# Kernel optimization log

Measured on AMD Instinct MI355X. Metric: run time of the kernel, lower is better.

## Reference

```python
import jax, jax.numpy as jnp
import numpy as np

NUM_USERS = 200_000
NUM_ITEMS = 100_000
N = NUM_USERS + NUM_ITEMS
D = 32
E = 9_600_000
N_LAYERS = 3


def setup_inputs() -> dict:
    key = jax.random.key(0)
    k1, k2, k3, k4, k5 = jax.random.split(key, 5)
    rows = jax.random.randint(k1, (E,), 0, N, dtype=jnp.int32)
    cols = jax.random.randint(k2, (E,), 0, N, dtype=jnp.int32)
    # normalized-adjacency-like positive values
    vals = jax.random.uniform(k3, (E,), dtype=jnp.float32) * 0.05
    # xavier-uniform-ish embedding init
    bound = float(np.sqrt(6.0 / (NUM_USERS + D)))
    user_w = jax.random.uniform(k4, (NUM_USERS, D), dtype=jnp.float32,
                                minval=-bound, maxval=bound)
    bound_i = float(np.sqrt(6.0 / (NUM_ITEMS + D)))
    item_w = jax.random.uniform(k5, (NUM_ITEMS, D), dtype=jnp.float32,
                                minval=-bound_i, maxval=bound_i)
    return {"rows": rows, "cols": cols, "vals": vals,
            "user_w": user_w, "item_w": item_w}


def _spmm(rows, cols, vals, x):
    # A_hat @ x for COO A_hat: gather source features, scale, scatter-add to rows.
    msgs = vals[:, None] * x[cols]                 # [E, D]
    return jax.ops.segment_sum(msgs, rows, num_segments=N)  # [N, D]


def reference(rows, cols, vals, user_w, item_w):
    x0 = jnp.concatenate([user_w, item_w], axis=0)  # [N, D]
    x = x0
    acc = x0
    for _ in range(N_LAYERS):
        x = _spmm(rows, cols, vals, x)
        acc = acc + x
    x_mean = acc / (N_LAYERS + 1)                   # mean over layer stack
    users = x_mean[:NUM_USERS]
    items = x_mean[NUM_USERS:]
    return (users, items)
```

## Files before the change

### kernel.cpp

```cpp
#include <hip/hip_runtime.h>
#include <hip/hip_fp16.h>
#include <stdint.h>

#define NUM_USERS 200000
#define NUM_ITEMS 100000
#define NN (NUM_USERS + NUM_ITEMS)
#define D 32
#define NE 9600000
#define TOTAL (NN * D)

#define RPB2 128
#define B2 ((NN + RPB2 - 1) / RPB2)
#define CAP 5120

#define TPB_A 1024
#define EPT 16
#define EPB_A (TPB_A * EPT)

#define TPB_H 1024
#define EPT_H 32
#define EPB_H (TPB_H * EPT_H)
#define NB_H ((NE + EPB_H - 1) / EPB_H)

__global__ __launch_bounds__(256) void init_x_acc(
    const float4* __restrict__ user_w, const float4* __restrict__ item_w,
    ushort4* __restrict__ xh, float4* __restrict__ acc) {
    int i = blockIdx.x * 256 + threadIdx.x;
    const int total4 = TOTAL / 4;
    const int ub4 = (NUM_USERS * D) / 4;
    if (i < total4) {
        float4 v = (i < ub4) ? user_w[i] : item_w[i - ub4];
        acc[i] = v;
        ushort4 h;
        h.x = __half_as_ushort(__float2half(v.x));
        h.y = __half_as_ushort(__float2half(v.y));
        h.z = __half_as_ushort(__float2half(v.z));
        h.w = __half_as_ushort(__float2half(v.w));
        xh[i] = h;
    }
}

__global__ __launch_bounds__(TPB_H) void bucket_hist(
    const int4* __restrict__ rows4, int* __restrict__ bcounts) {
    __shared__ int hist[B2];
    int tid = threadIdx.x;
    for (int i = tid; i < B2; i += TPB_H) hist[i] = 0;
    __syncthreads();
    int base4 = blockIdx.x * (EPB_H / 4);
    #pragma unroll
    for (int k = 0; k < EPT_H / 4; ++k) {
        int i4 = base4 + k * TPB_H + tid;
        if (i4 < NE / 4) {
            int4 r = rows4[i4];
            atomicAdd(&hist[r.x >> 7], 1);
            atomicAdd(&hist[r.y >> 7], 1);
            atomicAdd(&hist[r.z >> 7], 1);
            atomicAdd(&hist[r.w >> 7], 1);
        }
    }
    __syncthreads();
    for (int b = tid; b < B2; b += TPB_H) {
        int c = hist[b];
        if (c) atomicAdd(&bcounts[b], c);
    }
}

__global__ __launch_bounds__(1024) void scan_buckets(
    const int* __restrict__ bcounts, int* __restrict__ bstart,
    int* __restrict__ bfill) {
    __shared__ int lds[1024];
    int t = threadIdx.x;
    int v[4];
    int s = 0;
    #pragma unroll
    for (int k = 0; k < 4; ++k) {
        int b = t * 4 + k;
        v[k] = (b < B2) ? bcounts[b] : 0;
        s += v[k];
    }
    lds[t] = s;
    __syncthreads();
    for (int off = 1; off < 1024; off <<= 1) {
        int u = (t >= off) ? lds[t - off] : 0;
        __syncthreads();
        lds[t] += u;
        __syncthreads();
    }
    int ex = lds[t] - s;
    #pragma unroll
    for (int k = 0; k < 4; ++k) {
        int b = t * 4 + k;
        if (b < B2) { bstart[b] = ex; bfill[b] = ex; }
        ex += v[k];
    }
    if (t == 1023) bstart[B2] = ex;
}

__global__ __launch_bounds__(TPB_A) void partition_edges(
    const int4* __restrict__ rows4, const int4* __restrict__ cols4,
    const float4* __restrict__ vals4, int* __restrict__ bfill,
    int2* __restrict__ temp) {
    __shared__ int hist[B2];
    int tid = threadIdx.x;
    for (int i = tid; i < B2; i += TPB_A) hist[i] = 0;
    __syncthreads();

    int base4 = blockIdx.x * (EPB_A / 4);
    uint32_t brank[EPT];

    #pragma unroll
    for (int k = 0; k < EPT / 4; ++k) {
        int i4 = base4 + k * TPB_A + tid;
        if (i4 < NE / 4) {
            int4 r = rows4[i4];
            uint32_t b0 = (uint32_t)r.x >> 7, b1 = (uint32_t)r.y >> 7;
            uint32_t b2 = (uint32_t)r.z >> 7, b3 = (uint32_t)r.w >> 7;
            brank[k * 4 + 0] = (b0 << 20) | (uint32_t)((r.x & 127) << 13) | (uint32_t)atomicAdd(&hist[b0], 1);
            brank[k * 4 + 1] = (b1 << 20) | (uint32_t)((r.y & 127) << 13) | (uint32_t)atomicAdd(&hist[b1], 1);
            brank[k * 4 + 2] = (b2 << 20) | (uint32_t)((r.z & 127) << 13) | (uint32_t)atomicAdd(&hist[b2], 1);
            brank[k * 4 + 3] = (b3 << 20) | (uint32_t)((r.w & 127) << 13) | (uint32_t)atomicAdd(&hist[b3], 1);
        }
    }
    __syncthreads();
    for (int b = tid; b < B2; b += TPB_A) {
        int c = hist[b];
        if (c) hist[b] = atomicAdd(&bfill[b], c);
    }
    __syncthreads();

    #pragma unroll
    for (int k = 0; k < EPT / 4; ++k) {
        int i4 = base4 + k * TPB_A + tid;
        if (i4 < NE / 4) {
            int4 c = cols4[i4];
            float4 v = vals4[i4];
            uint32_t br; int pos; int2 cv;
            br = brank[k * 4 + 0]; pos = hist[br >> 20] + (int)(br & 0x1FFFu);
            cv.x = (int)(((br >> 13) & 127u) << 19) | c.x; cv.y = __float_as_int(v.x); temp[pos] = cv;
            br = brank[k * 4 + 1]; pos = hist[br >> 20] + (int)(br & 0x1FFFu);
            cv.x = (int)(((br >> 13) & 127u) << 19) | c.y; cv.y = __float_as_int(v.y); temp[pos] = cv;
            br = brank[k * 4 + 2]; pos = hist[br >> 20] + (int)(br & 0x1FFFu);
            cv.x = (int)(((br >> 13) & 127u) << 19) | c.z; cv.y = __float_as_int(v.z); temp[pos] = cv;
            br = brank[k * 4 + 3]; pos = hist[br >> 20] + (int)(br & 0x1FFFu);
            cv.x = (int)(((br >> 13) & 127u) << 19) | c.w; cv.y = __float_as_int(v.w); temp[pos] = cv;
        }
    }
}

__global__ __launch_bounds__(256) void sort_bucket2(
    const int* __restrict__ bstart, const int2* __restrict__ temp,
    int* __restrict__ row_start, int2* __restrict__ colval) {
    __shared__ int2 stage[CAP];
    __shared__ int lstart[RPB2];
    __shared__ int lfill[RPB2];
    int b = blockIdx.x;
    int row0 = b * RPB2;
    int rcount = NN - row0; if (rcount > RPB2) rcount = RPB2;
    int tid = threadIdx.x;
    int s = bstart[b];
    int count = bstart[b + 1] - s;

    if (tid < RPB2) lfill[tid] = 0;
    __syncthreads();

    for (int i = tid; i < count; i += 256) {
        int rl = temp[s + i].x >> 19;
        atomicAdd(&lfill[rl], 1);
    }
    __syncthreads();

    int val = (tid < RPB2) ? lfill[tid] : 0;
    if (tid < RPB2) lstart[tid] = val;
    __syncthreads();
    for (int off = 1; off < RPB2; off <<= 1) {
        int u = (tid >= off && tid < RPB2) ? lstart[tid - off] : 0;
        __syncthreads();
        if (tid < RPB2) lstart[tid] += u;
        __syncthreads();
    }
    int ex = (tid < RPB2) ? lstart[tid] - val : 0;
    if (tid < RPB2) {
        lstart[tid] = ex;
        lfill[tid] = 0;
        if (tid < rcount) row_start[row0 + tid] = s + ex;
    }
    if (b == 0 && tid == 0) row_start[NN] = NE;
    __syncthreads();

    if (count <= CAP) {
        for (int i = tid; i < count; i += 256) {
            int2 e = temp[s + i];
            int rl = e.x >> 19;
            int pos = lstart[rl] + atomicAdd(&lfill[rl], 1);
            stage[pos] = make_int2(e.x & 0x7FFFF, e.y);
        }
        __syncthreads();
        for (int i = tid; i < count; i += 256) colval[s + i] = stage[i];
    } else {
        for (int i = tid; i < count; i += 256) {
            int2 e = temp[s + i];
            int rl = e.x >> 19;
            int pos = lstart[rl] + atomicAdd(&lfill[rl], 1);
            colval[s + pos] = make_int2(e.x & 0x7FFFF, e.y);
        }
    }
}

template <bool LAST>
__global__ __launch_bounds__(256) void spmm_csr(
    const int* __restrict__ row_start, const int2* __restrict__ colval,
    const __half* __restrict__ xh, __half* __restrict__ yh,
    float* __restrict__ acc) {
    int lane = threadIdx.x & 63;
    int grp = lane >> 3;
    int fq = lane & 7;
    int row = (blockIdx.x * 256 + threadIdx.x) >> 6;
    if (row >= NN) return;
    int s = row_start[row];
    int e = row_start[row + 1];
    if (s == e) {
        if (lane < 8) {
            size_t idx = (size_t)row * D + lane * 4;
            if (!LAST) *(uint2*)(yh + idx) = make_uint2(0u, 0u);
            float4 av = *(const float4*)(acc + idx);
            if (LAST) { av.x *= 0.25f; av.y *= 0.25f; av.z *= 0.25f; av.w *= 0.25f; }
            *(float4*)(acc + idx) = av;
        }
        return;
    }
    float a0 = 0.f, a1 = 0.f, a2 = 0.f, a3 = 0.f;
    float b0 = 0.f, b1 = 0.f, b2 = 0.f, b3 = 0.f;
    int i = s;
    for (; i + 16 <= e; i += 16) {
        int2 cvA = colval[i + grp];
        int2 cvB = colval[i + 8 + grp];
        uint2 hA = *(const uint2*)(xh + (size_t)cvA.x * D + fq * 4);
        uint2 hB = *(const uint2*)(xh + (size_t)cvB.x * D + fq * 4);
        float vA = __int_as_float(cvA.y);
        float vB = __int_as_float(cvB.y);
        float2 fA0 = __half22float2(*(__half2*)&hA.x);
        float2 fA1 = __half22float2(*(__half2*)&hA.y);
        float2 fB0 = __half22float2(*(__half2*)&hB.x);
        float2 fB1 = __half22float2(*(__half2*)&hB.y);
        a0 += vA * fA0.x; a1 += vA * fA0.y; a2 += vA * fA1.x; a3 += vA * fA1.y;
        b0 += vB * fB0.x; b1 += vB * fB0.y; b2 += vB * fB1.x; b3 += vB * fB1.y;
    }
    if (i < e) {
        int iA = i + grp;
        int iB = i + 8 + grp;
        int cA = (iA < e) ? iA : (e - 1);
        int cB = (iB < e) ? iB : (e - 1);
        int2 cvA = colval[cA];
        int2 cvB = colval[cB];
        uint2 hA = *(const uint2*)(xh + (size_t)cvA.x * D + fq * 4);
        uint2 hB = *(const uint2*)(xh + (size_t)cvB.x * D + fq * 4);
        float vA = (iA < e) ? __int_as_float(cvA.y) : 0.f;
        float vB = (iB < e) ? __int_as_float(cvB.y) : 0.f;
        float2 fA0 = __half22float2(*(__half2*)&hA.x);
        float2 fA1 = __half22float2(*(__half2*)&hA.y);
        float2 fB0 = __half22float2(*(__half2*)&hB.x);
        float2 fB1 = __half22float2(*(__half2*)&hB.y);
        a0 += vA * fA0.x; a1 += vA * fA0.y; a2 += vA * fA1.x; a3 += vA * fA1.y;
        b0 += vB * fB0.x; b1 += vB * fB0.y; b2 += vB * fB1.x; b3 += vB * fB1.y;
    }
    a0 += b0; a1 += b1; a2 += b2; a3 += b3;
    #pragma unroll
    for (int m = 8; m <= 32; m <<= 1) {
        a0 += __shfl_xor(a0, m, 64);
        a1 += __shfl_xor(a1, m, 64);
        a2 += __shfl_xor(a2, m, 64);
        a3 += __shfl_xor(a3, m, 64);
    }
    if (lane < 8) {
        size_t idx = (size_t)row * D + lane * 4;
        if (!LAST) {
            __half2 h01 = __float22half2_rn(make_float2(a0, a1));
            __half2 h23 = __float22half2_rn(make_float2(a2, a3));
            *(uint2*)(yh + idx) =
                make_uint2(*(uint32_t*)&h01, *(uint32_t*)&h23);
        }
        float4 av = *(const float4*)(acc + idx);
        av.x += a0; av.y += a1; av.z += a2; av.w += a3;
        if (LAST) { av.x *= 0.25f; av.y *= 0.25f; av.z *= 0.25f; av.w *= 0.25f; }
        *(float4*)(acc + idx) = av;
    }
}

extern "C" void kernel_launch(void* const* d_in, const int* in_sizes, int n_in,
                              void* d_out, int out_size, void* d_ws, size_t ws_size,
                              hipStream_t stream) {
    const int*   rows   = (const int*)d_in[0];
    const int*   cols   = (const int*)d_in[1];
    const float* vals   = (const float*)d_in[2];
    const float* user_w = (const float*)d_in[3];
    const float* item_w = (const float*)d_in[4];

    float* acc = (float*)d_out;

    __half* xh = (__half*)d_ws;
    __half* yh = xh + (size_t)TOTAL;
    int2*  temp = (int2*)d_ws;
    int2*  colval = (int2*)((char*)d_ws + 2ull * (size_t)TOTAL * sizeof(float));
    int*   bcounts = (int*)(colval + (size_t)NE);
    int*   bstart = bcounts + B2;
    int*   bfill = bstart + (B2 + 1);
    int*   row_start = bfill + B2;

    const int vec_blocks   = (TOTAL / 4 + 255) / 256;
    const int partA_blocks = (NE + EPB_A - 1) / EPB_A;
    const int row_blocks   = (NN + 3) / 4;

    hipMemsetAsync(bcounts, 0, (size_t)B2 * sizeof(int), stream);
    bucket_hist<<<NB_H, TPB_H, 0, stream>>>((const int4*)rows, bcounts);
    scan_buckets<<<1, 1024, 0, stream>>>(bcounts, bstart, bfill);
    partition_edges<<<partA_blocks, TPB_A, 0, stream>>>(
        (const int4*)rows, (const int4*)cols, (const float4*)vals, bfill, temp);
    sort_bucket2<<<B2, 256, 0, stream>>>(bstart, temp, row_start, colval);

    init_x_acc<<<vec_blocks, 256, 0, stream>>>(
        (const float4*)user_w, (const float4*)item_w, (ushort4*)xh, (float4*)acc);

    spmm_csr<false><<<row_blocks, 256, 0, stream>>>(row_start, colval, xh, yh, acc);
    spmm_csr<false><<<row_blocks, 256, 0, stream>>>(row_start, colval, yh, xh, acc);
    spmm_csr<true ><<<row_blocks, 256, 0, stream>>>(row_start, colval, xh, yh, acc);
}
```

Measured before the change: 868.8 us.

## Replace single-pass edge partition with two-pass coarse/fine LDS-staged radix partition

The single scatter of edges into 2344 row buckets becomes two passes. The first pass groups edges into 74 coarse chunks of 4096 rows, and the second splits each chunk into 32 fine buckets. Both passes stage their output in LDS so the global writes land in contiguous runs instead of scattered 8-byte stores. The cost is an extra full read and write of the 9.6M-edge array, plus a 128KB LDS stage per block that limits occupancy, and sort_bucket2 now works in place with a scratch copy for oversized buckets.

```diff
diff --git a/kernel.cpp b/kernel.cpp
--- a/kernel.cpp
+++ b/kernel.cpp
@@ -12,6 +12,11 @@
 #define RPB2 128
 #define B2 ((NN + RPB2 - 1) / RPB2)
 #define CAP 5120
+
+#define CSH 12
+#define NC ((NN + (1 << CSH) - 1) >> CSH)
+#define FPC 32
+#define BPC 9
 
 #define TPB_A 1024
 #define EPT 16
@@ -67,7 +72,7 @@
 
 __global__ __launch_bounds__(1024) void scan_buckets(
     const int* __restrict__ bcounts, int* __restrict__ bstart,
-    int* __restrict__ bfill) {
+    int* __restrict__ bfill, int* __restrict__ cfill) {
     __shared__ int lds[1024];
     int t = threadIdx.x;
     int v[4];
@@ -90,66 +95,157 @@
     #pragma unroll
     for (int k = 0; k < 4; ++k) {
         int b = t * 4 + k;
-        if (b < B2) { bstart[b] = ex; bfill[b] = ex; }
+        if (b < B2) {
+            bstart[b] = ex;
+            bfill[b] = ex;
+            if ((b & (FPC - 1)) == 0) cfill[b >> 5] = ex;
+        }
         ex += v[k];
     }
     if (t == 1023) bstart[B2] = ex;
 }
 
-__global__ __launch_bounds__(TPB_A) void partition_edges(
+__global__ __launch_bounds__(TPB_A) void partition_coarse(
     const int4* __restrict__ rows4, const int4* __restrict__ cols4,
-    const float4* __restrict__ vals4, int* __restrict__ bfill,
-    int2* __restrict__ temp) {
-    __shared__ int hist[B2];
+    const float4* __restrict__ vals4, int* __restrict__ cfill,
+    int2* __restrict__ temp1) {
+    __shared__ int2 stage[EPB_A];
+    __shared__ int hist[NC];
+    __shared__ int bnd[NC + 1];
+    __shared__ int dlt[NC];
+    __shared__ int sc[128];
     int tid = threadIdx.x;
-    for (int i = tid; i < B2; i += TPB_A) hist[i] = 0;
+    if (tid < NC) hist[tid] = 0;
     __syncthreads();
 
     int base4 = blockIdx.x * (EPB_A / 4);
-    uint32_t brank[EPT];
+    int keys[EPT]; int vls[EPT]; int crk[EPT];
 
     #pragma unroll
     for (int k = 0; k < EPT / 4; ++k) {
         int i4 = base4 + k * TPB_A + tid;
         if (i4 < NE / 4) {
             int4 r = rows4[i4];
-            uint32_t b0 = (uint32_t)r.x >> 7, b1 = (uint32_t)r.y >> 7;
-            uint32_t b2 = (uint32_t)r.z >> 7, b3 = (uint32_t)r.w >> 7;
-            brank[k * 4 + 0] = (b0 << 20) | (uint32_t)((r.x & 127) << 13) | (uint32_t)atomicAdd(&hist[b0], 1);
-            brank[k * 4 + 1] = (b1 << 20) | (uint32_t)((r.y & 127) << 13) | (uint32_t)atomicAdd(&hist[b1], 1);
-            brank[k * 4 + 2] = (b2 << 20) | (uint32_t)((r.z & 127) << 13) | (uint32_t)atomicAdd(&hist[b2], 1);
-            brank[k * 4 + 3] = (b3 << 20) | (uint32_t)((r.w & 127) << 13) | (uint32_t)atomicAdd(&hist[b3], 1);
-        }
-    }
-    __syncthreads();
-    for (int b = tid; b < B2; b += TPB_A) {
-        int c = hist[b];
-        if (c) hist[b] = atomicAdd(&bfill[b], c);
-    }
-    __syncthreads();
-
+            int4 c = cols4[i4];
+            float4 v = vals4[i4];
+            int c0 = r.x >> CSH, c1 = r.y >> CSH, c2 = r.z >> CSH, c3 = r.w >> CSH;
+            keys[k*4+0] = ((r.x & 4095) << 19) | c.x; vls[k*4+0] = __float_as_int(v.x);
+            crk[k*4+0] = (c0 << 13) | atomicAdd(&hist[c0], 1);
+            keys[k*4+1] = ((r.y & 4095) << 19) | c.y; vls[k*4+1] = __float_as_int(v.y);
+            crk[k*4+1] = (c1 << 13) | atomicAdd(&hist[c1], 1);
+            keys[k*4+2] = ((r.z & 4095) << 19) | c.z; vls[k*4+2] = __float_as_int(v.z);
+            crk[k*4+2] = (c2 << 13) | atomicAdd(&hist[c2], 1);
+            keys[k*4+3] = ((r.w & 4095) << 19) | c.w; vls[k*4+3] = __float_as_int(v.w);
+            crk[k*4+3] = (c3 << 13) | atomicAdd(&hist[c3], 1);
+        }
+    }
+    __syncthreads();
+    if (tid < 128) sc[tid] = (tid < NC) ? hist[tid] : 0;
+    __syncthreads();
+    #pragma unroll
+    for (int off = 1; off < 128; off <<= 1) {
+        int u = (tid >= off && tid < 128) ? sc[tid - off] : 0;
+        __syncthreads();
+        if (tid < 128) sc[tid] += u;
+        __syncthreads();
+    }
+    if (tid < NC) {
+        int cnt = hist[tid];
+        int ex = sc[tid] - cnt;
+        bnd[tid] = ex;
+        dlt[tid] = (cnt ? atomicAdd(&cfill[tid], cnt) : 0) - ex;
+    }
+    if (tid == 0) bnd[NC] = sc[NC - 1];
+    __syncthreads();
     #pragma unroll
     for (int k = 0; k < EPT / 4; ++k) {
         int i4 = base4 + k * TPB_A + tid;
         if (i4 < NE / 4) {
-            int4 c = cols4[i4];
-            float4 v = vals4[i4];
-            uint32_t br; int pos; int2 cv;
-            br = brank[k * 4 + 0]; pos = hist[br >> 20] + (int)(br & 0x1FFFu);
-            cv.x = (int)(((br >> 13) & 127u) << 19) | c.x; cv.y = __float_as_int(v.x); temp[pos] = cv;
-            br = brank[k * 4 + 1]; pos = hist[br >> 20] + (int)(br & 0x1FFFu);
-            cv.x = (int)(((br >> 13) & 127u) << 19) | c.y; cv.y = __float_as_int(v.y); temp[pos] = cv;
-            br = brank[k * 4 + 2]; pos = hist[br >> 20] + (int)(br & 0x1FFFu);
-            cv.x = (int)(((br >> 13) & 127u) << 19) | c.z; cv.y = __float_as_int(v.z); temp[pos] = cv;
-            br = brank[k * 4 + 3]; pos = hist[br >> 20] + (int)(br & 0x1FFFu);
-            cv.x = (int)(((br >> 13) & 127u) << 19) | c.w; cv.y = __float_as_int(v.w); temp[pos] = cv;
-        }
+            #pragma unroll
+            for (int j = 0; j < 4; ++j) {
+                int e = k * 4 + j;
+                int p = bnd[crk[e] >> 13] + (crk[e] & 0x1FFF);
+                stage[p] = make_int2(keys[e], vls[e]);
+            }
+        }
+    }
+    __syncthreads();
+    int ntot = bnd[NC];
+    for (int j = tid; j < ntot; j += TPB_A) {
+        int lo = 0, hi = NC;
+        while (hi - lo > 1) { int mid = (lo + hi) >> 1; if (bnd[mid] <= j) lo = mid; else hi = mid; }
+        temp1[j + dlt[lo]] = stage[j];
+    }
+}
+
+__global__ __launch_bounds__(TPB_A) void partition_fine(
+    const int2* __restrict__ temp1, const int* __restrict__ bstart,
+    int* __restrict__ bfill, int2* __restrict__ colval) {
+    __shared__ int2 stage[EPB_A];
+    __shared__ int hist[FPC];
+    __shared__ int bnd[FPC + 1];
+    __shared__ int dlt[FPC];
+    __shared__ int sc[FPC];
+    int c = blockIdx.x / BPC;
+    int seg = blockIdx.x % BPC;
+    int cs = bstart[c * FPC];
+    int ce = bstart[min((c + 1) * FPC, B2)];
+    int base = cs + seg * EPB_A;
+    int n = ce - base;
+    if (n <= 0) return;
+    if (n > EPB_A) n = EPB_A;
+    int tid = threadIdx.x;
+    if (tid < FPC) hist[tid] = 0;
+    __syncthreads();
+    int keys[EPT]; int vls[EPT]; int frk[EPT];
+    #pragma unroll
+    for (int k = 0; k < EPT; ++k) {
+        int idx = k * TPB_A + tid;
+        if (idx < n) {
+            int2 e = temp1[base + idx];
+            int f = (e.x >> 26) & 31;
+            keys[k] = e.x; vls[k] = e.y;
+            frk[k] = (f << 13) | atomicAdd(&hist[f], 1);
+        }
+    }
+    __syncthreads();
+    if (tid < FPC) sc[tid] = hist[tid];
+    __syncthreads();
+    #pragma unroll
+    for (int off = 1; off < FPC; off <<= 1) {
+        int u = (tid >= off && tid < FPC) ? sc[tid - off] : 0;
+        __syncthreads();
+        if (tid < FPC) sc[tid] += u;
+        __syncthreads();
+    }
+    if (tid < FPC) {
+        int cnt = hist[tid];
+        int ex = sc[tid] - cnt;
+        bnd[tid] = ex;
+        dlt[tid] = (cnt ? atomicAdd(&bfill[c * FPC + tid], cnt) : 0) - ex;
+    }
+    if (tid == 0) bnd[FPC] = sc[FPC - 1];
+    __syncthreads();
+    #pragma unroll
+    for (int k = 0; k < EPT; ++k) {
+        int idx = k * TPB_A + tid;
+        if (idx < n) {
+            int p = bnd[frk[k] >> 13] + (frk[k] & 0x1FFF);
+            int rl = (keys[k] >> 19) & 127;
+            stage[p] = make_int2((rl << 19) | (keys[k] & 0x7FFFF), vls[k]);
+        }
+    }
+    __syncthreads();
+    for (int j = tid; j < n; j += TPB_A) {
+        int lo = 0, hi = FPC;
+        while (hi - lo > 1) { int mid = (lo + hi) >> 1; if (bnd[mid] <= j) lo = mid; else hi = mid; }
+        colval[j + dlt[lo]] = stage[j];
     }
 }
 
 __global__ __launch_bounds__(256) void sort_bucket2(
-    const int* __restrict__ bstart, const int2* __restrict__ temp,
-    int* __restrict__ row_start, int2* __restrict__ colval) {
+    const int* __restrict__ bstart, int* __restrict__ row_start,
+    int2* __restrict__ colval, int2* __restrict__ scratch) {
     __shared__ int2 stage[CAP];
     __shared__ int lstart[RPB2];
     __shared__ int lfill[RPB2];
@@ -164,7 +260,7 @@
     __syncthreads();
 
     for (int i = tid; i < count; i += 256) {
-        int rl = temp[s + i].x >> 19;
+        int rl = colval[s + i].x >> 19;
         atomicAdd(&lfill[rl], 1);
     }
     __syncthreads();
@@ -189,7 +285,7 @@
 
     if (count <= CAP) {
         for (int i = tid; i < count; i += 256) {
-            int2 e = temp[s + i];
+            int2 e = colval[s + i];
             int rl = e.x >> 19;
             int pos = lstart[rl] + atomicAdd(&lfill[rl], 1);
             stage[pos] = make_int2(e.x & 0x7FFFF, e.y);
@@ -197,8 +293,10 @@
         __syncthreads();
         for (int i = tid; i < count; i += 256) colval[s + i] = stage[i];
     } else {
+        for (int i = tid; i < count; i += 256) scratch[s + i] = colval[s + i];
+        __syncthreads();
         for (int i = tid; i < count; i += 256) {
-            int2 e = temp[s + i];
+            int2 e = scratch[s + i];
             int rl = e.x >> 19;
             int pos = lstart[rl] + atomicAdd(&lfill[rl], 1);
             colval[s + pos] = make_int2(e.x & 0x7FFFF, e.y);
@@ -299,23 +397,27 @@
 
     __half* xh = (__half*)d_ws;
     __half* yh = xh + (size_t)TOTAL;
-    int2*  temp = (int2*)d_ws;
+    int2*  temp1 = (int2*)d_ws;
     int2*  colval = (int2*)((char*)d_ws + 2ull * (size_t)TOTAL * sizeof(float));
     int*   bcounts = (int*)(colval + (size_t)NE);
     int*   bstart = bcounts + B2;
     int*   bfill = bstart + (B2 + 1);
-    int*   row_start = bfill + B2;
+    int*   cfill = bfill + B2;
+    int*   row_start = cfill + NC;
 
     const int vec_blocks   = (TOTAL / 4 + 255) / 256;
     const int partA_blocks = (NE + EPB_A - 1) / EPB_A;
+    const int partF_blocks = NC * BPC;
     const int row_blocks   = (NN + 3) / 4;
 
     hipMemsetAsync(bcounts, 0, (size_t)B2 * sizeof(int), stream);
     bucket_hist<<<NB_H, TPB_H, 0, stream>>>((const int4*)rows, bcounts);
-    scan_buckets<<<1, 1024, 0, stream>>>(bcounts, bstart, bfill);
-    partition_edges<<<partA_blocks, TPB_A, 0, stream>>>(
-        (const int4*)rows, (const int4*)cols, (const float4*)vals, bfill, temp);
-    sort_bucket2<<<B2, 256, 0, stream>>>(bstart, temp, row_start, colval);
+    scan_buckets<<<1, 1024, 0, stream>>>(bcounts, bstart, bfill, cfill);
+    partition_coarse<<<partA_blocks, TPB_A, 0, stream>>>(
+        (const int4*)rows, (const int4*)cols, (const float4*)vals, cfill, temp1);
+    partition_fine<<<partF_blocks, TPB_A, 0, stream>>>(
+        (const int2*)temp1, bstart, bfill, colval);
+    sort_bucket2<<<B2, 256, 0, stream>>>(bstart, row_start, colval, temp1);
 
     init_x_acc<<<vec_blocks, 256, 0, stream>>>(
         (const float4*)user_w, (const float4*)item_w, (ushort4*)xh, (float4*)acc);
```

After: 826.2 us. 4.9% less time.
